# Kernel optimization log

Measured on AMD Instinct MI355X. Metric: run time of the kernel, lower is better.

## Reference

```python
import jax, jax.numpy as jnp
import numpy as np

EMB_DIM = 128
MID = 192  # ceil(1.5 * emb_dim)
VOCAB = 3000
KCLS = 5
B = 16
S = 128
EPS = 1e-5


def _linear_init(k, fin, fout):
    k1, k2 = jax.random.split(k)
    bound = 1.0 / np.sqrt(fin)
    W = jax.random.uniform(k1, (fin, fout), minval=-bound, maxval=bound, dtype=jnp.float32)
    b = jax.random.uniform(k2, (fout,), minval=-bound, maxval=bound, dtype=jnp.float32)
    return W, b


def setup_inputs() -> dict:
    key = jax.random.key(0)
    ks = jax.random.split(key, 7)
    emb = jax.random.normal(ks[0], (VOCAB, EMB_DIM), dtype=jnp.float32)
    W1, b1 = _linear_init(ks[1], 2 * EMB_DIM, MID)   # encoder layer 1
    W2, b2 = _linear_init(ks[2], MID, EMB_DIM)       # encoder layer 2
    W3, b3 = _linear_init(ks[3], EMB_DIM, MID)       # decoder layer 1
    W4, b4 = _linear_init(ks[4], MID, 2 * EMB_DIM)   # decoder layer 2
    Wk, bk = _linear_init(ks[5], EMB_DIM, KCLS)      # soft head
    inputs = jax.random.randint(ks[6], (B, S), 0, VOCAB, dtype=jnp.int64)
    return dict(inputs=inputs, emb=emb, W1=W1, b1=b1, W2=W2, b2=b2,
                W3=W3, b3=b3, W4=W4, b4=b4, Wk=Wk, bk=bk)


def _forward(inputs, emb, W1, b1, W2, b2, W3, b3, W4, b4, Wk, bk):
    X = emb[inputs]                      # (B,S,m)
    Bs, Sl, m = X.shape
    bidx = jnp.arange(Bs)
    karr = jnp.arange(Sl)
    jarr = jnp.arange(Sl - 1)

    def step(carry, t):
        nodes, counts, acc = carry       # (B,S,m), (B,S), (B,)
        L = Sl - t                       # current active list length
        right, left = nodes[:, 1:], nodes[:, :-1]          # pair j = (node[j+1], node[j])
        y = (jnp.concatenate([right, left], -1) @ W1 + b1) @ W2 + b2   # (B,S-1,m)
        xx = (y @ W3 + b3) @ W4 + b4                                    # (B,S-1,2m)
        # torch cross_entropy with float-vector target: -sum(target * log_softmax(input))
        ls1 = -(right * jax.nn.log_softmax(xx[..., :m], -1)).sum(-1)
        ls2 = -(left * jax.nn.log_softmax(xx[..., m:], -1)).sum(-1)
        n1, n2 = counts[:, 1:], counts[:, :-1]
        loss = ((n1 + EPS) * ls1 + (n2 + EPS) * ls2) / (n1 + n2 + EPS)
        valid = jarr < (L - 1)                                          # only first L-1 pairs active
        idx = jnp.argmin(jnp.where(valid[None, :], loss, jnp.inf), axis=1)  # (B,)
        acc = acc + jnp.take_along_axis(loss, idx[:, None], 1)[:, 0]
        father_x = jnp.take_along_axis(y, idx[:, None, None], 1)[:, 0]  # (B,m)
        # faithful bug: lc = nodelist[idx-1] (python wrap to L-1 when idx==0), rc = nodelist[idx]
        lc_idx = jnp.where(idx == 0, L - 1, idx - 1)
        father_cnt = (jnp.take_along_axis(counts, idx[:, None], 1)[:, 0]
                      + jnp.take_along_axis(counts, lc_idx[:, None], 1)[:, 0])
        pos = jnp.maximum(idx - 1, 0)
        # new list: drop lc and rc, father lands at pos; gather map reproduces list insert/remove
        src = jnp.where((idx[:, None] == 0) | (karr[None, :] < idx[:, None] - 1),
                        karr[None, :], karr[None, :] + 1)
        src = jnp.minimum(src, Sl - 1)
        nodes = jnp.take_along_axis(nodes, src[:, :, None], 1).at[bidx, pos].set(father_x)
        counts = jnp.take_along_axis(counts, src, 1).at[bidx, pos].set(father_cnt)
        return (nodes, counts, acc), None

    init = (X, jnp.ones((Bs, Sl), X.dtype), jnp.zeros((Bs,), X.dtype))
    (nodes, counts, acc), _ = jax.lax.scan(step, init, jnp.arange(Sl - 1))
    pred = jnp.argmax(nodes[:, 0] @ Wk + bk, axis=-1)   # argmax softmax == argmax logits
    return pred, acc.sum() / Bs


def reference(inputs, emb, W1, b1, W2, b2, W3, b3, W4, b4, Wk, bk):
    return _forward(inputs, emb, W1, b1, W2, b2, W3, b3, W4, b4, Wk, bk)
```

## Files before the change

### kernel.cpp

```cpp
#include <hip/hip_runtime.h>
#include <math.h>

#define EMB 128
#define MID 192
#define SEQ 128
#define BATCH 16
#define NPAIR 127
#define KCLS 5
#define EPSF 1e-5f

#define OFF_WYT   0
#define OFF_BY    32768
#define OFF_WXXT  32896
#define OFF_BXX   65664
#define OFF_NODES 65920
#define OFF_YC    328064
#define OFF_L0    588160

__global__ void k_comp(const float* __restrict__ W1, const float* __restrict__ b1,
                       const float* __restrict__ W2, const float* __restrict__ b2,
                       const float* __restrict__ W3, const float* __restrict__ b3,
                       const float* __restrict__ W4, const float* __restrict__ b4,
                       float* __restrict__ ws) {
    int tid = blockIdx.x * blockDim.x + threadIdx.x;
    if (tid < 32768) {
        int k = tid >> 7, o = tid & 127;
        float a = 0.f;
        for (int j = 0; j < MID; ++j) a += W1[k*MID+j] * W2[j*EMB+o];
        int q = k >> 6, jj = k & 63;
        ws[OFF_WYT + (size_t)(o*4 + q)*64 + jj] = a;
    } else if (tid < 65536) {
        int t = tid - 32768;
        int k = t >> 8, c = t & 255;
        float a = 0.f;
        for (int j = 0; j < MID; ++j) a += W3[k*MID+j] * W4[j*256+c];
        int hh = k >> 6, jj = k & 63;
        ws[OFF_WXXT + (size_t)(c*2 + hh)*64 + jj] = a;
    } else if (tid < 65536 + 128) {
        int o = tid - 65536;
        float a = b2[o];
        for (int j = 0; j < MID; ++j) a += b1[j] * W2[j*EMB+o];
        ws[OFF_BY + o] = a;
    } else if (tid < 65536 + 128 + 256) {
        int o = tid - 65536 - 128;
        float a = b4[o];
        for (int j = 0; j < MID; ++j) a += b3[j] * W4[j*256+o];
        ws[OFF_BXX + o] = a;
    }
}

__global__ void k_nodes(const int* __restrict__ inp, const float* __restrict__ emb,
                        float* __restrict__ ws) {
    int tid = blockIdx.x * blockDim.x + threadIdx.x;
    if (tid >= BATCH*SEQ*EMB) return;
    int d = tid & 127;
    int bs = tid >> 7;
    int tok = inp[bs];
    ws[OFF_NODES + tid] = emb[tok*EMB + d];
}

__global__ void __launch_bounds__(512, 1) k_init(float* __restrict__ ws) {
    __shared__ float s_x[2][2*EMB];
    __shared__ float s_red[4][2][EMB];
    __shared__ float s_redx[2][2][256];
    __shared__ float s_y[2][EMB];
    __shared__ float s_by[EMB];
    __shared__ float s_bxx[2*EMB];
    __shared__ float s_ls[2][2];
    int tid = threadIdx.x;
    int b = blockIdx.x >> 3, g = blockIdx.x & 7;
    float wy[64], wxx[64];
    {
        const float4* gw = (const float4*)(ws + OFF_WYT) + ((size_t)(tid & 127)*4 + (tid >> 7))*16;
        #pragma unroll
        for (int i = 0; i < 16; ++i) { float4 v = gw[i]; wy[4*i]=v.x; wy[4*i+1]=v.y; wy[4*i+2]=v.z; wy[4*i+3]=v.w; }
        const float4* gx = (const float4*)(ws + OFF_WXXT) + ((size_t)(tid & 255)*2 + (tid >> 8))*16;
        #pragma unroll
        for (int i = 0; i < 16; ++i) { float4 v = gx[i]; wxx[4*i]=v.x; wxx[4*i+1]=v.y; wxx[4*i+2]=v.z; wxx[4*i+3]=v.w; }
    }
    if (tid < EMB) s_by[tid] = ws[OFF_BY + tid];
    if (tid < 2*EMB) s_bxx[tid] = ws[OFF_BXX + tid];
    const float* nodes = ws + OFF_NODES + (size_t)b*SEQ*EMB;
    float* yc = ws + OFF_YC + (size_t)b*NPAIR*EMB;
    int q4 = tid >> 7, o = tid & 127;
    int hh = tid >> 8, c = tid & 255;
    int p_s = tid >> 8, kk = tid & 255;
    __syncthreads();
    for (int i = 0; i < 8; ++i) {
        int base = g*16 + i*2;
        {
            int j = base + p_s;
            int jj = j < NPAIR ? j : NPAIR - 1;
            s_x[p_s][kk] = nodes[(jj + (kk < 128 ? 1 : 0))*EMB + (kk & 127)];
        }
        __syncthreads();
        float a0 = 0.f, a1 = 0.f;
        #pragma unroll
        for (int j = 0; j < 64; ++j) {
            float w = wy[j];
            a0 += s_x[0][q4*64 + j] * w;
            a1 += s_x[1][q4*64 + j] * w;
        }
        s_red[q4][0][o] = a0;
        s_red[q4][1][o] = a1;
        __syncthreads();
        if (tid < 256) {
            int p = tid >> 7, oo = tid & 127;
            float yv = s_red[0][p][oo] + s_red[1][p][oo] + s_red[2][p][oo] + s_red[3][p][oo] + s_by[oo];
            s_y[p][oo] = yv;
            int j2 = base + p;
            if (j2 < NPAIR) yc[(size_t)j2*EMB + oo] = yv;
        }
        __syncthreads();
        float c0 = 0.f, c1 = 0.f;
        #pragma unroll
        for (int j = 0; j < 64; ++j) {
            float w = wxx[j];
            c0 += s_y[0][hh*64 + j] * w;
            c1 += s_y[1][hh*64 + j] * w;
        }
        s_redx[hh][0][c] = c0;
        s_redx[hh][1][c] = c1;
        __syncthreads();
        if (tid < 256) {
            int w = tid >> 6, lane = tid & 63;
            int p2 = w >> 1, h2 = w & 1;
            int cA = h2*128 + lane, cB = cA + 64;
            float v0 = s_redx[0][p2][cA] + s_redx[1][p2][cA] + s_bxx[cA];
            float v1 = s_redx[0][p2][cB] + s_redx[1][p2][cB] + s_bxx[cB];
            float m = fmaxf(v0, v1);
            for (int s = 32; s; s >>= 1) m = fmaxf(m, __shfl_xor(m, s, 64));
            float se = expf(v0 - m) + expf(v1 - m);
            for (int s = 32; s; s >>= 1) se += __shfl_xor(se, s, 64);
            float lse = m + logf(se);
            float o0 = s_x[p2][cA], o1 = s_x[p2][cB];
            float term = o0*(v0 - lse) + o1*(v1 - lse);
            for (int s = 32; s; s >>= 1) term += __shfl_xor(term, s, 64);
            if (lane == 0) s_ls[p2][h2] = -term;
        }
        __syncthreads();
        if (tid < 2) {
            int j2 = base + tid;
            if (j2 < NPAIR) {
                float l = ((1.f+EPSF)*s_ls[tid][0] + (1.f+EPSF)*s_ls[tid][1]) / (2.f + EPSF);
                ws[OFF_L0 + b*NPAIR + j2] = l;
            }
        }
        __syncthreads();
    }
}

#define SX(p, c) s_x[p][(((c) >> 6)*72) + ((c) & 63)]

__global__ void __launch_bounds__(512, 1) k_seq(float* __restrict__ ws,
                      const float* __restrict__ Wk, const float* __restrict__ bkv,
                      float* __restrict__ out) {
    __shared__ float s_nodes[SEQ*EMB];
    __shared__ float s_yc[NPAIR*EMB];
    __shared__ float s_x[2][4*72];
    __shared__ float s_y[2][EMB];
    __shared__ float s_xx[2][2*EMB];
    __shared__ float s_by[EMB];
    __shared__ float s_bxx[2*EMB];
    __shared__ float s_ls[2][2];
    __shared__ float s_loss[2][SEQ];
    __shared__ float s_cnt[2][SEQ];
    __shared__ int   s_nslot[2][SEQ];
    __shared__ int   s_yslot[2][SEQ];
    __shared__ float s_restv[2];
    __shared__ int   s_resti[2];
    __shared__ float s_log[KCLS];

    int tid = threadIdx.x;
    int b = blockIdx.x;
    float wy[64], wxx[64];
    {
        const float4* gw = (const float4*)(ws + OFF_WYT) + (size_t)tid*16;
        #pragma unroll
        for (int i = 0; i < 16; ++i) { float4 v = gw[i]; wy[4*i]=v.x; wy[4*i+1]=v.y; wy[4*i+2]=v.z; wy[4*i+3]=v.w; }
        const float4* gx = (const float4*)(ws + OFF_WXXT) + (size_t)tid*16;
        #pragma unroll
        for (int i = 0; i < 16; ++i) { float4 v = gx[i]; wxx[4*i]=v.x; wxx[4*i+1]=v.y; wxx[4*i+2]=v.z; wxx[4*i+3]=v.w; }
    }
    {
        const float4* gn = (const float4*)(ws + OFF_NODES + (size_t)b*SEQ*EMB);
        float4* sn = (float4*)s_nodes;
        for (int i = tid; i < SEQ*EMB/4; i += 512) sn[i] = gn[i];
        const float4* gy = (const float4*)(ws + OFF_YC + (size_t)b*NPAIR*EMB);
        float4* sy = (float4*)s_yc;
        for (int i = tid; i < NPAIR*EMB/4; i += 512) sy[i] = gy[i];
    }
    if (tid < EMB) s_by[tid] = ws[OFF_BY + tid];
    if (tid < 2*EMB) s_bxx[tid] = ws[OFF_BXX + tid];
    if (tid < NPAIR) { s_loss[0][tid] = ws[OFF_L0 + b*NPAIR + tid]; s_yslot[0][tid] = tid; }
    if (tid < SEQ)   { s_cnt[0][tid] = 1.f; s_nslot[0][tid] = tid; }

    float acc = 0.f;
    int cur = 0;
    int q0c = -1, q1c = -1;
    int slotFr = 0, ysIr = 0, myslot = 0;
    bool stageYc = false;
    const int q4 = tid & 3,  oy = tid >> 2;
    const int hh = tid & 1,  cx = tid >> 1;
    const int sp = tid >> 8, skk = tid & 255;
    __syncthreads();

    #pragma unroll 1
    for (int t = 0; t < NPAIR; ++t) {
        const int L = SEQ - t;
        if (t > 0) {
            if (tid < EMB) s_nodes[slotFr*EMB + tid] = s_yc[(size_t)ysIr*EMB + tid];
            {
                float xv = stageYc ? s_yc[(size_t)ysIr*EMB + (skk & 127)]
                                   : s_nodes[myslot*EMB + (skk & 127)];
                s_x[sp][((skk >> 6)*72) + (skk & 63)] = xv;
            }
            __syncthreads();
            {
                float a0 = 0.f, a1 = 0.f;
                const float* x0 = &s_x[0][q4*72];
                const float* x1 = &s_x[1][q4*72];
                #pragma unroll
                for (int j = 0; j < 64; ++j) { float w = wy[j]; a0 += x0[j]*w; a1 += x1[j]*w; }
                a0 += __shfl_xor(a0, 1, 64); a1 += __shfl_xor(a1, 1, 64);
                a0 += __shfl_xor(a0, 2, 64); a1 += __shfl_xor(a1, 2, 64);
                if (q4 == 0) {
                    float bb = s_by[oy];
                    float y0 = a0 + bb, y1 = a1 + bb;
                    s_y[0][oy] = y0; s_y[1][oy] = y1;
                    s_yc[(size_t)s_yslot[cur][q0c]*EMB + oy] = y0;
                    s_yc[(size_t)s_yslot[cur][q1c]*EMB + oy] = y1;
                }
            }
            __syncthreads();
            {
                float c0 = 0.f, c1 = 0.f;
                const float* y0p = &s_y[0][hh*64];
                const float* y1p = &s_y[1][hh*64];
                #pragma unroll
                for (int j = 0; j < 64; ++j) { float w = wxx[j]; c0 += y0p[j]*w; c1 += y1p[j]*w; }
                c0 += __shfl_xor(c0, 1, 64); c1 += __shfl_xor(c1, 1, 64);
                if (hh == 0) {
                    float bb = s_bxx[cx];
                    s_xx[0][cx] = c0 + bb;
                    s_xx[1][cx] = c1 + bb;
                }
            }
            __syncthreads();
        }
        if (t > 0 && tid < 128) {
            int p2 = tid >> 6, h2 = (tid >> 5) & 1, l5 = tid & 31;
            int base = h2*128 + l5;
            float v0 = s_xx[p2][base],      v1 = s_xx[p2][base+32];
            float v2 = s_xx[p2][base+64],   v3 = s_xx[p2][base+96];
            float o0 = SX(p2, base),        o1 = SX(p2, base+32);
            float o2 = SX(p2, base+64),     o3 = SX(p2, base+96);
            float m   = fmaxf(fmaxf(v0, v1), fmaxf(v2, v3));
            float sov = v0*o0 + v1*o1 + v2*o2 + v3*o3;
            float so  = (o0 + o1) + (o2 + o3);
            for (int s = 16; s; s >>= 1) {
                m    = fmaxf(m, __shfl_xor(m, s, 64));
                sov += __shfl_xor(sov, s, 64);
                so  += __shfl_xor(so, s, 64);
            }
            float se = expf(v0 - m) + expf(v1 - m) + expf(v2 - m) + expf(v3 - m);
            for (int s = 16; s; s >>= 1) se += __shfl_xor(se, s, 64);
            if (l5 == 0) s_ls[p2][h2] = (m + logf(se))*so - sov;
        } else if (tid >= 128 && tid < 256) {
            int j = tid - 128;
            float v = (j <= L-2 && j != q0c && j != q1c) ? s_loss[cur][j] : INFINITY;
            int ii = j;
            for (int s = 32; s; s >>= 1) {
                float ov = __shfl_xor(v, s, 64);
                int   oi = __shfl_xor(ii, s, 64);
                if (ov < v || (ov == v && oi < ii)) { v = ov; ii = oi; }
            }
            if ((tid & 63) == 0) { s_restv[(tid >> 6) - 2] = v; s_resti[(tid >> 6) - 2] = ii; }
        }
        __syncthreads();
        float l0 = INFINITY, l1 = INFINITY;
        if (t > 0) {
            float n1a = s_cnt[cur][q0c+1], n2a = s_cnt[cur][q0c];
            l0 = ((n1a + EPSF)*s_ls[0][0] + (n2a + EPSF)*s_ls[0][1]) / (n1a + n2a + EPSF);
            float n1b = s_cnt[cur][q1c+1], n2b = s_cnt[cur][q1c];
            l1 = ((n1b + EPSF)*s_ls[1][0] + (n2b + EPSF)*s_ls[1][1]) / (n1b + n2b + EPSF);
        }
        float bv = s_restv[0]; int bi = s_resti[0];
        {
            float rv = s_restv[1]; int ri = s_resti[1];
            if (rv < bv || (rv == bv && ri < bi)) { bv = rv; bi = ri; }
        }
        if (t > 0) {
            if (l1 < bv || (l1 == bv && q1c < bi)) { bv = l1; bi = q1c; }
            if (l0 < bv || (l0 == bv && q0c < bi)) { bv = l0; bi = q0c; }
        }
        if (tid == 0) acc += bv;
        const int idx = bi;
        const int pos = idx > 0 ? idx - 1 : 0;
        const bool dS = idx > 0;
        const float fcnt = s_cnt[cur][idx] + s_cnt[cur][idx == 0 ? L-1 : idx-1];
        slotFr = s_nslot[cur][pos];
        ysIr   = s_yslot[cur][idx];
        const int nxt = cur ^ 1;
        if (tid < NPAIR) {
            int sh = (dS && tid >= pos+1 && tid <= L-3) ? 1 : 0;
            int sj = tid + sh;
            float v = (sj == q0c) ? l0 : (sj == q1c) ? l1 : s_loss[cur][sj];
            s_loss[nxt][tid]  = v;
            s_yslot[nxt][tid] = s_yslot[cur][sj];
        }
        if (tid < SEQ) {
            int sh = (dS && tid >= pos+1 && tid <= L-2) ? 1 : 0;
            s_cnt[nxt][tid]   = (tid == pos) ? fcnt : s_cnt[cur][tid + sh];
            s_nslot[nxt][tid] = s_nslot[cur][tid + sh];
        }
        q0c = pos >= 1 ? pos - 1 : 0;
        q1c = pos;
        {
            int qq = (sp ? q1c : q0c) + (skk < 128 ? 1 : 0);
            stageYc = (qq == q1c);
            int sh = (dS && qq >= pos+1 && qq <= L-2) ? 1 : 0;
            myslot = s_nslot[cur][qq + sh];
        }
        cur = nxt;
        __syncthreads();
    }
    {
        int w = tid >> 6, l = tid & 63;
        if (w < KCLS) {
            const float* root = s_yc + (size_t)ysIr*EMB;
            float p = root[2*l]*Wk[(2*l)*KCLS + w] + root[2*l+1]*Wk[(2*l+1)*KCLS + w];
            for (int s = 32; s; s >>= 1) p += __shfl_xor(p, s, 64);
            if (l == 0) s_log[w] = p + bkv[w];
        }
    }
    __syncthreads();
    if (tid == 0) {
        int best = 0;
        for (int cc = 1; cc < KCLS; ++cc) if (s_log[cc] > s_log[best]) best = cc;
        out[b] = (float)best;
        atomicAdd(&out[BATCH], acc * (1.f/16.f));
    }
}

extern "C" void kernel_launch(void* const* d_in, const int* in_sizes, int n_in,
                              void* d_out, int out_size, void* d_ws, size_t ws_size,
                              hipStream_t stream) {
    const int*   inp = (const int*)d_in[0];
    const float* emb = (const float*)d_in[1];
    const float* W1  = (const float*)d_in[2];
    const float* b1  = (const float*)d_in[3];
    const float* W2  = (const float*)d_in[4];
    const float* b2  = (const float*)d_in[5];
    const float* W3  = (const float*)d_in[6];
    const float* b3  = (const float*)d_in[7];
    const float* W4  = (const float*)d_in[8];
    const float* b4  = (const float*)d_in[9];
    const float* Wk  = (const float*)d_in[10];
    const float* bk  = (const float*)d_in[11];
    float* out = (float*)d_out;
    float* ws  = (float*)d_ws;

    hipMemsetAsync(d_out, 0, (size_t)out_size * sizeof(float), stream);

    k_comp<<<(65920 + 255) / 256, 256, 0, stream>>>(W1, b1, W2, b2, W3, b3, W4, b4, ws);
    k_nodes<<<(BATCH*SEQ*EMB + 255) / 256, 256, 0, stream>>>(inp, emb, ws);
    k_init<<<BATCH * 8, 512, 0, stream>>>(ws);
    k_seq<<<BATCH, 512, 0, stream>>>(ws, Wk, bk, out);
}
```

Measured before the change: 539.0 us.

## Move node and pair caches to global memory and stage weights in LDS

The per-batch node list and cached pair outputs (s_nodes, s_yc) move out of shared memory into the global workspace. The freed LDS holds the first-layer weight rows (padded to 68 floats per thread), which used to live in registers. The second-layer weights are now reloaded from global as float4s at every step. The aim is to cut register pressure from the two 64-float per-thread weight arrays, at the cost of global-memory round trips and cross-thread global visibility inside a strictly sequential 127-step loop.

```diff
diff --git a/kernel.cpp b/kernel.cpp
--- a/kernel.cpp
+++ b/kernel.cpp
@@ -152,11 +152,16 @@
 
 #define SX(p, c) s_x[p][(((c) >> 6)*72) + ((c) & 63)]
 
+#define S2G(P, base) \
+    c0 = fmaf(y0p[(base)+0], P.x, c0); c1 = fmaf(y1p[(base)+0], P.x, c1); \
+    c0 = fmaf(y0p[(base)+1], P.y, c0); c1 = fmaf(y1p[(base)+1], P.y, c1); \
+    c0 = fmaf(y0p[(base)+2], P.z, c0); c1 = fmaf(y1p[(base)+2], P.z, c1); \
+    c0 = fmaf(y0p[(base)+3], P.w, c0); c1 = fmaf(y1p[(base)+3], P.w, c1);
+
 __global__ void __launch_bounds__(512, 1) k_seq(float* __restrict__ ws,
                       const float* __restrict__ Wk, const float* __restrict__ bkv,
                       float* __restrict__ out) {
-    __shared__ float s_nodes[SEQ*EMB];
-    __shared__ float s_yc[NPAIR*EMB];
+    __shared__ float s_wy[512*68];
     __shared__ float s_x[2][4*72];
     __shared__ float s_y[2][EMB];
     __shared__ float s_xx[2][2*EMB];
@@ -173,22 +178,15 @@
 
     int tid = threadIdx.x;
     int b = blockIdx.x;
-    float wy[64], wxx[64];
+    float* gn  = ws + OFF_NODES + (size_t)b*SEQ*EMB;
+    float* gyc = ws + OFF_YC   + (size_t)b*NPAIR*EMB;
+    const float4* gxx = (const float4*)(ws + OFF_WXXT) + (size_t)tid*16;
+
     {
         const float4* gw = (const float4*)(ws + OFF_WYT) + (size_t)tid*16;
-        #pragma unroll
-        for (int i = 0; i < 16; ++i) { float4 v = gw[i]; wy[4*i]=v.x; wy[4*i+1]=v.y; wy[4*i+2]=v.z; wy[4*i+3]=v.w; }
-        const float4* gx = (const float4*)(ws + OFF_WXXT) + (size_t)tid*16;
-        #pragma unroll
-        for (int i = 0; i < 16; ++i) { float4 v = gx[i]; wxx[4*i]=v.x; wxx[4*i+1]=v.y; wxx[4*i+2]=v.z; wxx[4*i+3]=v.w; }
-    }
-    {
-        const float4* gn = (const float4*)(ws + OFF_NODES + (size_t)b*SEQ*EMB);
-        float4* sn = (float4*)s_nodes;
-        for (int i = tid; i < SEQ*EMB/4; i += 512) sn[i] = gn[i];
-        const float4* gy = (const float4*)(ws + OFF_YC + (size_t)b*NPAIR*EMB);
-        float4* sy = (float4*)s_yc;
-        for (int i = tid; i < NPAIR*EMB/4; i += 512) sy[i] = gy[i];
+        float4* dst = (float4*)(s_wy + (size_t)tid*68);
+        #pragma unroll
+        for (int i = 0; i < 16; ++i) dst[i] = gw[i];
     }
     if (tid < EMB) s_by[tid] = ws[OFF_BY + tid];
     if (tid < 2*EMB) s_bxx[tid] = ws[OFF_BXX + tid];
@@ -203,16 +201,21 @@
     const int q4 = tid & 3,  oy = tid >> 2;
     const int hh = tid & 1,  cx = tid >> 1;
     const int sp = tid >> 8, skk = tid & 255;
+    const float* wrow = s_wy + (size_t)tid*68;
     __syncthreads();
 
     #pragma unroll 1
     for (int t = 0; t < NPAIR; ++t) {
         const int L = SEQ - t;
         if (t > 0) {
-            if (tid < EMB) s_nodes[slotFr*EMB + tid] = s_yc[(size_t)ysIr*EMB + tid];
+            float4 P0 = gxx[0],  P1 = gxx[1],  P2 = gxx[2],  P3 = gxx[3];
+            float4 P4 = gxx[4],  P5 = gxx[5],  P6 = gxx[6],  P7 = gxx[7];
+            float4 P8 = gxx[8],  P9 = gxx[9],  P10 = gxx[10], P11 = gxx[11];
+            float4 P12 = gxx[12], P13 = gxx[13], P14 = gxx[14], P15 = gxx[15];
+            if (tid < EMB) gn[slotFr*EMB + tid] = gyc[(size_t)ysIr*EMB + tid];
             {
-                float xv = stageYc ? s_yc[(size_t)ysIr*EMB + (skk & 127)]
-                                   : s_nodes[myslot*EMB + (skk & 127)];
+                float xv = stageYc ? gyc[(size_t)ysIr*EMB + (skk & 127)]
+                                   : gn[(size_t)myslot*EMB + (skk & 127)];
                 s_x[sp][((skk >> 6)*72) + (skk & 63)] = xv;
             }
             __syncthreads();
@@ -221,15 +224,19 @@
                 const float* x0 = &s_x[0][q4*72];
                 const float* x1 = &s_x[1][q4*72];
                 #pragma unroll
-                for (int j = 0; j < 64; ++j) { float w = wy[j]; a0 += x0[j]*w; a1 += x1[j]*w; }
+                for (int j = 0; j < 64; ++j) {
+                    float w = wrow[j];
+                    a0 = fmaf(x0[j], w, a0);
+                    a1 = fmaf(x1[j], w, a1);
+                }
                 a0 += __shfl_xor(a0, 1, 64); a1 += __shfl_xor(a1, 1, 64);
                 a0 += __shfl_xor(a0, 2, 64); a1 += __shfl_xor(a1, 2, 64);
                 if (q4 == 0) {
                     float bb = s_by[oy];
                     float y0 = a0 + bb, y1 = a1 + bb;
                     s_y[0][oy] = y0; s_y[1][oy] = y1;
-                    s_yc[(size_t)s_yslot[cur][q0c]*EMB + oy] = y0;
-                    s_yc[(size_t)s_yslot[cur][q1c]*EMB + oy] = y1;
+                    gyc[(size_t)s_yslot[cur][q0c]*EMB + oy] = y0;
+                    gyc[(size_t)s_yslot[cur][q1c]*EMB + oy] = y1;
                 }
             }
             __syncthreads();
@@ -237,8 +244,10 @@
                 float c0 = 0.f, c1 = 0.f;
                 const float* y0p = &s_y[0][hh*64];
                 const float* y1p = &s_y[1][hh*64];
-                #pragma unroll
-                for (int j = 0; j < 64; ++j) { float w = wxx[j]; c0 += y0p[j]*w; c1 += y1p[j]*w; }
+                S2G(P0, 0)   S2G(P1, 4)   S2G(P2, 8)   S2G(P3, 12)
+                S2G(P4, 16)  S2G(P5, 20)  S2G(P6, 24)  S2G(P7, 28)
+                S2G(P8, 32)  S2G(P9, 36)  S2G(P10, 40) S2G(P11, 44)
+                S2G(P12, 48) S2G(P13, 52) S2G(P14, 56) S2G(P15, 60)
                 c0 += __shfl_xor(c0, 1, 64); c1 += __shfl_xor(c1, 1, 64);
                 if (hh == 0) {
                     float bb = s_bxx[cx];
@@ -328,7 +337,7 @@
     {
         int w = tid >> 6, l = tid & 63;
         if (w < KCLS) {
-            const float* root = s_yc + (size_t)ysIr*EMB;
+            const float* root = gyc + (size_t)ysIr*EMB;
             float p = root[2*l]*Wk[(2*l)*KCLS + w] + root[2*l+1]*Wk[(2*l+1)*KCLS + w];
             for (int s = 32; s; s >>= 1) p += __shfl_xor(p, s, 64);
             if (l == 0) s_log[w] = p + bkv[w];
```

Result: slower. 1.010 ms (+87.3%).

## Use DPP/swizzle reductions and fold staging into the update phase, removing a barrier

Applied to the files above, without the earlier changes.

Replaces __shfl_xor cross-lane reductions in the matvec, log-softmax and argmin stages with DPP row operations and ds_swizzle. The argmin now reduces within 32-lane groups into four partial slots. The father-node write and the s_x staging for the next step move to the end of the previous iteration, before its trailing barrier. This drops one __syncthreads per step of the 127-step sequential loop. It adds explicit fmaf, relies on DPP control encodings being correct, and changes how the final root node is located.

```diff
diff --git a/kernel.cpp b/kernel.cpp
--- a/kernel.cpp
+++ b/kernel.cpp
@@ -59,6 +59,11 @@
     ws[OFF_NODES + tid] = emb[tok*EMB + d];
 }
 
+#define DPPF(x, ctrl) __int_as_float(__builtin_amdgcn_update_dpp(0, __float_as_int(x), (ctrl), 0xF, 0xF, true))
+#define DPPI(x, ctrl) __builtin_amdgcn_update_dpp(0, (x), (ctrl), 0xF, 0xF, true)
+#define SWZ16F(x) __int_as_float(__builtin_amdgcn_ds_swizzle(__float_as_int(x), 0x401F))
+#define SWZ16I(x) __builtin_amdgcn_ds_swizzle((x), 0x401F)
+
 __global__ void __launch_bounds__(512, 1) k_init(float* __restrict__ ws) {
     __shared__ float s_x[2][2*EMB];
     __shared__ float s_red[4][2][EMB];
@@ -167,8 +172,8 @@
     __shared__ float s_cnt[2][SEQ];
     __shared__ int   s_nslot[2][SEQ];
     __shared__ int   s_yslot[2][SEQ];
-    __shared__ float s_restv[2];
-    __shared__ int   s_resti[2];
+    __shared__ float s_restv[4];
+    __shared__ int   s_resti[4];
     __shared__ float s_log[KCLS];
 
     int tid = threadIdx.x;
@@ -198,8 +203,6 @@
     float acc = 0.f;
     int cur = 0;
     int q0c = -1, q1c = -1;
-    int slotFr = 0, ysIr = 0, myslot = 0;
-    bool stageYc = false;
     const int q4 = tid & 3,  oy = tid >> 2;
     const int hh = tid & 1,  cx = tid >> 1;
     const int sp = tid >> 8, skk = tid & 255;
@@ -209,21 +212,14 @@
     for (int t = 0; t < NPAIR; ++t) {
         const int L = SEQ - t;
         if (t > 0) {
-            if (tid < EMB) s_nodes[slotFr*EMB + tid] = s_yc[(size_t)ysIr*EMB + tid];
-            {
-                float xv = stageYc ? s_yc[(size_t)ysIr*EMB + (skk & 127)]
-                                   : s_nodes[myslot*EMB + (skk & 127)];
-                s_x[sp][((skk >> 6)*72) + (skk & 63)] = xv;
-            }
-            __syncthreads();
             {
                 float a0 = 0.f, a1 = 0.f;
                 const float* x0 = &s_x[0][q4*72];
                 const float* x1 = &s_x[1][q4*72];
                 #pragma unroll
-                for (int j = 0; j < 64; ++j) { float w = wy[j]; a0 += x0[j]*w; a1 += x1[j]*w; }
-                a0 += __shfl_xor(a0, 1, 64); a1 += __shfl_xor(a1, 1, 64);
-                a0 += __shfl_xor(a0, 2, 64); a1 += __shfl_xor(a1, 2, 64);
+                for (int j = 0; j < 64; ++j) { float w = wy[j]; a0 = fmaf(x0[j], w, a0); a1 = fmaf(x1[j], w, a1); }
+                a0 += DPPF(a0, 0xB1); a1 += DPPF(a1, 0xB1);
+                a0 += DPPF(a0, 0x4E); a1 += DPPF(a1, 0x4E);
                 if (q4 == 0) {
                     float bb = s_by[oy];
                     float y0 = a0 + bb, y1 = a1 + bb;
@@ -238,8 +234,8 @@
                 const float* y0p = &s_y[0][hh*64];
                 const float* y1p = &s_y[1][hh*64];
                 #pragma unroll
-                for (int j = 0; j < 64; ++j) { float w = wxx[j]; c0 += y0p[j]*w; c1 += y1p[j]*w; }
-                c0 += __shfl_xor(c0, 1, 64); c1 += __shfl_xor(c1, 1, 64);
+                for (int j = 0; j < 64; ++j) { float w = wxx[j]; c0 = fmaf(y0p[j], w, c0); c1 = fmaf(y1p[j], w, c1); }
+                c0 += DPPF(c0, 0xB1); c1 += DPPF(c1, 0xB1);
                 if (hh == 0) {
                     float bb = s_bxx[cx];
                     s_xx[0][cx] = c0 + bb;
@@ -258,24 +254,33 @@
             float m   = fmaxf(fmaxf(v0, v1), fmaxf(v2, v3));
             float sov = v0*o0 + v1*o1 + v2*o2 + v3*o3;
             float so  = (o0 + o1) + (o2 + o3);
-            for (int s = 16; s; s >>= 1) {
-                m    = fmaxf(m, __shfl_xor(m, s, 64));
-                sov += __shfl_xor(sov, s, 64);
-                so  += __shfl_xor(so, s, 64);
-            }
+            m = fmaxf(m, DPPF(m, 0xB1));  sov += DPPF(sov, 0xB1);  so += DPPF(so, 0xB1);
+            m = fmaxf(m, DPPF(m, 0x4E));  sov += DPPF(sov, 0x4E);  so += DPPF(so, 0x4E);
+            m = fmaxf(m, DPPF(m, 0x124)); sov += DPPF(sov, 0x124); so += DPPF(so, 0x124);
+            m = fmaxf(m, DPPF(m, 0x128)); sov += DPPF(sov, 0x128); so += DPPF(so, 0x128);
+            m = fmaxf(m, SWZ16F(m));      sov += SWZ16F(sov);      so += SWZ16F(so);
             float se = expf(v0 - m) + expf(v1 - m) + expf(v2 - m) + expf(v3 - m);
-            for (int s = 16; s; s >>= 1) se += __shfl_xor(se, s, 64);
+            se += DPPF(se, 0xB1);
+            se += DPPF(se, 0x4E);
+            se += DPPF(se, 0x124);
+            se += DPPF(se, 0x128);
+            se += SWZ16F(se);
             if (l5 == 0) s_ls[p2][h2] = (m + logf(se))*so - sov;
         } else if (tid >= 128 && tid < 256) {
             int j = tid - 128;
             float v = (j <= L-2 && j != q0c && j != q1c) ? s_loss[cur][j] : INFINITY;
             int ii = j;
-            for (int s = 32; s; s >>= 1) {
-                float ov = __shfl_xor(v, s, 64);
-                int   oi = __shfl_xor(ii, s, 64);
-                if (ov < v || (ov == v && oi < ii)) { v = ov; ii = oi; }
-            }
-            if ((tid & 63) == 0) { s_restv[(tid >> 6) - 2] = v; s_resti[(tid >> 6) - 2] = ii; }
+            {   float ov = DPPF(v, 0xB1);  int oi = DPPI(ii, 0xB1);
+                bool tk = (ov < v) || (ov == v && oi < ii); v = tk ? ov : v; ii = tk ? oi : ii; }
+            {   float ov = DPPF(v, 0x4E);  int oi = DPPI(ii, 0x4E);
+                bool tk = (ov < v) || (ov == v && oi < ii); v = tk ? ov : v; ii = tk ? oi : ii; }
+            {   float ov = DPPF(v, 0x124); int oi = DPPI(ii, 0x124);
+                bool tk = (ov < v) || (ov == v && oi < ii); v = tk ? ov : v; ii = tk ? oi : ii; }
+            {   float ov = DPPF(v, 0x128); int oi = DPPI(ii, 0x128);
+                bool tk = (ov < v) || (ov == v && oi < ii); v = tk ? ov : v; ii = tk ? oi : ii; }
+            {   float ov = SWZ16F(v);      int oi = SWZ16I(ii);
+                bool tk = (ov < v) || (ov == v && oi < ii); v = tk ? ov : v; ii = tk ? oi : ii; }
+            if ((j & 31) == 0) { s_restv[j >> 5] = v; s_resti[j >> 5] = ii; }
         }
         __syncthreads();
         float l0 = INFINITY, l1 = INFINITY;
@@ -286,8 +291,9 @@
             l1 = ((n1b + EPSF)*s_ls[1][0] + (n2b + EPSF)*s_ls[1][1]) / (n1b + n2b + EPSF);
         }
         float bv = s_restv[0]; int bi = s_resti[0];
-        {
-            float rv = s_restv[1]; int ri = s_resti[1];
+        #pragma unroll
+        for (int g = 1; g < 4; ++g) {
+            float rv = s_restv[g]; int ri = s_resti[g];
             if (rv < bv || (rv == bv && ri < bi)) { bv = rv; bi = ri; }
         }
         if (t > 0) {
@@ -299,8 +305,8 @@
         const int pos = idx > 0 ? idx - 1 : 0;
         const bool dS = idx > 0;
         const float fcnt = s_cnt[cur][idx] + s_cnt[cur][idx == 0 ? L-1 : idx-1];
-        slotFr = s_nslot[cur][pos];
-        ysIr   = s_yslot[cur][idx];
+        const int slotFr = s_nslot[cur][pos];
+        const int ysIr   = s_yslot[cur][idx];
         const int nxt = cur ^ 1;
         if (tid < NPAIR) {
             int sh = (dS && tid >= pos+1 && tid <= L-3) ? 1 : 0;
@@ -316,11 +322,15 @@
         }
         q0c = pos >= 1 ? pos - 1 : 0;
         q1c = pos;
+        if (tid < EMB) s_nodes[slotFr*EMB + tid] = s_yc[(size_t)ysIr*EMB + tid];
         {
             int qq = (sp ? q1c : q0c) + (skk < 128 ? 1 : 0);
-            stageYc = (qq == q1c);
+            bool sYc = (qq == q1c);
             int sh = (dS && qq >= pos+1 && qq <= L-2) ? 1 : 0;
-            myslot = s_nslot[cur][qq + sh];
+            int ms = s_nslot[cur][qq + sh];
+            float xv = sYc ? s_yc[(size_t)ysIr*EMB + (skk & 127)]
+                           : s_nodes[(size_t)ms*EMB + (skk & 127)];
+            s_x[sp][((skk >> 6)*72) + (skk & 63)] = xv;
         }
         cur = nxt;
         __syncthreads();
@@ -328,7 +338,7 @@
     {
         int w = tid >> 6, l = tid & 63;
         if (w < KCLS) {
-            const float* root = s_yc + (size_t)ysIr*EMB;
+            const float* root = s_nodes + (size_t)s_nslot[cur][0]*EMB;
             float p = root[2*l]*Wk[(2*l)*KCLS + w] + root[2*l+1]*Wk[(2*l+1)*KCLS + w];
             for (int s = 32; s; s >>= 1) p += __shfl_xor(p, s, 64);
             if (l == 0) s_log[w] = p + bkv[w];
```

Result: faster. 504.9 us (-6.3%).
